# Kernel optimization log

Measured on AMD Instinct MI355X. Metric: run time of the kernel, lower is better.

The kernel has to match this reference:

```python
import jax, jax.numpy as jnp
import numpy as np

N, C, HD = 8192, 1024, 128

def setup_inputs() -> dict:
    key = jax.random.key(0)
    ks = jax.random.split(key, 9)
    def xavier(k, fan_in, fan_out):
        lim = float(np.sqrt(6.0 / (fan_in + fan_out)))
        return jax.random.uniform(k, (fan_out, fan_in), jnp.float32, -lim, lim)
    return {
        "x": jax.random.normal(ks[0], (N, C), jnp.float32),
        "Wq": xavier(ks[1], C, HD), "bq": jnp.zeros((HD,), jnp.float32),
        "Wk": xavier(ks[2], C, HD), "bk": jnp.zeros((HD,), jnp.float32),
        "Wv": xavier(ks[3], C, C),  "bv": jnp.zeros((C,), jnp.float32),
        "Wo": xavier(ks[4], C, C),  "bo": jnp.zeros((C,), jnp.float32),
    }

def reference(x, Wq, bq, Wk, bk, Wv, bv, Wo, bo):
    scale = HD ** -0.5
    q = x @ Wq.T + bq          # (N, HD)
    k = x @ Wk.T + bk          # (N, HD)
    v = x @ Wv.T + bv          # (N, C)
    scores = (q @ k.T) * scale # (N, N)
    attn = jax.nn.softmax(scores, axis=-1)
    out = attn @ v             # (N, C)
    return out @ Wo.T + bo
```

## Files before the change

### kernel.cpp

```cpp
#include <hip/hip_runtime.h>

#define NTOK 8192
#define CDIM 1024
#define HDIM 128

typedef __attribute__((ext_vector_type(8))) short short8;
typedef __attribute__((ext_vector_type(4))) float floatx4;
typedef __attribute__((ext_vector_type(16))) float floatx16;

__device__ inline unsigned short f2bf(float f) {
    union { float f; unsigned u; } v; v.f = f;
    unsigned r = v.u + 0x7fffu + ((v.u >> 16) & 1u);
    return (unsigned short)(r >> 16);
}
__device__ inline float bf2f(short s) {
    union { unsigned u; float f; } v;
    v.u = ((unsigned)(unsigned short)s) << 16;
    return v.f;
}
__device__ inline void async16(const unsigned short* g, short* l) {
    __builtin_amdgcn_global_load_lds(
        (const __attribute__((address_space(1))) unsigned*)g,
        (__attribute__((address_space(3))) unsigned*)l, 16, 0, 0);
}

__global__ void cast_f32_bf16(const float* __restrict__ in,
                              unsigned short* __restrict__ out, int n4) {
    int i = blockIdx.x * blockDim.x + threadIdx.x;
    if (i < n4) {
        float4 v = ((const float4*)in)[i];
        ushort4 o;
        o.x = f2bf(v.x); o.y = f2bf(v.y); o.z = f2bf(v.z); o.w = f2bf(v.w);
        ((ushort4*)out)[i] = o;
    }
}

template<int SWZ>
__global__ __launch_bounds__(256) void gemm_nt(
    const unsigned short* __restrict__ A, const unsigned short* __restrict__ W,
    const float* __restrict__ bias, unsigned short* __restrict__ out, int M, int N, int K)
{
    __shared__ short As[4][64][8];
    __shared__ short Ws[4][64][8];
    const int tid = threadIdx.x;
    const int wave = tid >> 6, lane = tid & 63;
    const int lr = lane & 15, lc = lane >> 4;
    const int m0 = blockIdx.x * 64, n0 = blockIdx.y * 64;

    floatx4 acc[4] = {};
    const int srow = tid >> 2, sch = tid & 3;
    const unsigned short* Ag = A + (long)(m0 + srow) * K + sch * 8;
    const unsigned short* Wg = W + (long)(n0 + srow) * K + sch * 8;

    for (int k0 = 0; k0 < K; k0 += 32) {
        *(short8*)&As[sch][srow][0] = *(const short8*)(Ag + k0);
        *(short8*)&Ws[sch][srow][0] = *(const short8*)(Wg + k0);
        __syncthreads();
        short8 a = *(short8*)&As[lc][wave * 16 + lr][0];
#pragma unroll
        for (int s = 0; s < 4; s++) {
            short8 b = *(short8*)&Ws[lc][s * 16 + lr][0];
            acc[s] = __builtin_amdgcn_mfma_f32_16x16x32_bf16(a, b, acc[s], 0, 0, 0);
        }
        __syncthreads();
    }

#pragma unroll
    for (int s = 0; s < 4; s++) {
        int h = n0 + s * 16 + lr;
        float bv = bias[h];
        int tok0 = m0 + wave * 16 + lc * 4;
#pragma unroll
        for (int r = 0; r < 4; r++) {
            int tok = tok0 + r;
            if (SWZ)
                out[(tok >> 5) * 4096 + (h >> 3) * 256 + (tok & 31) * 8 + (h & 7)] =
                    f2bf(acc[s][r] + bv);
            else
                out[(long)tok * N + h] = f2bf(acc[s][r] + bv);
        }
    }
}

template<int MODE>
__global__ __launch_bounds__(256) void gemm128_nt(
    const unsigned short* __restrict__ A, const unsigned short* __restrict__ W,
    const float* __restrict__ bias, void* __restrict__ out, int M, int N, int K)
{
    __shared__ short As[128][4][8];
    __shared__ short Ws[128][4][8];
    const int tid = threadIdx.x, wave = tid >> 6, lane = tid & 63;
    const int lr = lane & 15, lc = lane >> 4;
    const int wm = (wave >> 1) * 64, wn = (wave & 1) * 64;
    const int m0 = blockIdx.x * 128, n0 = blockIdx.y * 128;

    floatx4 acc[4][4] = {};

    const int srow = lane >> 2, sch = lane & 3;
    const unsigned short* Ag0 = A + (long)(m0 + wave * 32 + srow) * K + sch * 8;
    const unsigned short* Ag1 = Ag0 + (long)16 * K;
    const unsigned short* Wg0 = W + (long)(n0 + wave * 32 + srow) * K + sch * 8;
    const unsigned short* Wg1 = Wg0 + (long)16 * K;
    short* lA0 = &As[wave * 32][0][0];
    short* lA1 = &As[wave * 32 + 16][0][0];
    short* lW0 = &Ws[wave * 32][0][0];
    short* lW1 = &Ws[wave * 32 + 16][0][0];

    for (int k0 = 0; k0 < K; k0 += 32) {
        async16(Ag0 + k0, lA0);
        async16(Ag1 + k0, lA1);
        async16(Wg0 + k0, lW0);
        async16(Wg1 + k0, lW1);
        __syncthreads();
        short8 af[4], bfg[4];
#pragma unroll
        for (int i = 0; i < 4; i++) af[i]  = *(short8*)&As[wm + i * 16 + lr][lc][0];
#pragma unroll
        for (int j = 0; j < 4; j++) bfg[j] = *(short8*)&Ws[wn + j * 16 + lr][lc][0];
#pragma unroll
        for (int i = 0; i < 4; i++)
#pragma unroll
            for (int j = 0; j < 4; j++)
                acc[i][j] = __builtin_amdgcn_mfma_f32_16x16x32_bf16(af[i], bfg[j], acc[i][j], 0, 0, 0);
        __syncthreads();
    }

#pragma unroll
    for (int i = 0; i < 4; i++) {
        int t0 = m0 + wm + i * 16 + lc * 4;
#pragma unroll
        for (int j = 0; j < 4; j++) {
            int c = n0 + wn + j * 16 + lr;
            float bv = bias[c];
            if (MODE == 0) {
                float* o = (float*)out;
#pragma unroll
                for (int r = 0; r < 4; r++) o[(long)(t0 + r) * N + c] = acc[i][j][r] + bv;
            } else {
                unsigned short* o = (unsigned short*)out;
                ushort4 pk;
                pk.x = f2bf(acc[i][j][0] + bv); pk.y = f2bf(acc[i][j][1] + bv);
                pk.z = f2bf(acc[i][j][2] + bv); pk.w = f2bf(acc[i][j][3] + bv);
                long off = (long)(c >> 8) * 2097152 + (t0 >> 5) * 8192 +
                           ((t0 & 31) >> 3) * 2048 + (c & 255) * 8 + (t0 & 7);
                *(ushort4*)&o[off] = pk;
            }
        }
    }
}

__global__ __launch_bounds__(256, 2) void attn_pv(
    const unsigned short* __restrict__ qb, const unsigned short* __restrict__ ksw,
    const unsigned short* __restrict__ vsw,
    unsigned short* __restrict__ Oa, unsigned short* __restrict__ Ob,
    float* __restrict__ la, float* __restrict__ lb)
{
    __shared__ short Ks[3][16][32][8];
    __shared__ short Vs[3][4][256][8];

    const int tid = threadIdx.x, wave = tid >> 6, lane = tid & 63;
    const int l31 = lane & 31, h = lane >> 5;
    const int m0 = blockIdx.x * 128, cblk = blockIdx.y;
    const int mw = m0 + wave * 32;
    const int nt0 = blockIdx.z * 128;
    unsigned short* Op = blockIdx.z ? Ob : Oa;
    float* ls = blockIdx.z ? lb : la;
    const float cexp = (float)(0.08838834764831845 * 1.4426950408889634);

    short8 qf[8];
#pragma unroll
    for (int kk = 0; kk < 8; kk++)
        qf[kk] = *(const short8*)&qb[(mw + l31) * HDIM + kk * 16 + h * 8];

    floatx16 acc[8] = {};
    float ls0 = 0.f, ls1 = 0.f, ls2 = 0.f, ls3 = 0.f;

    const unsigned short* kg[2];
#pragma unroll
    for (int t = 0; t < 2; t++) kg[t] = ksw + (wave * 2 + t) * 512 + lane * 8;
    const unsigned short* vg[4];
#pragma unroll
    for (int t = 0; t < 4; t++)
        vg[t] = vsw + (long)cblk * 2097152 + (wave * 4 + t) * 512 + lane * 8;

    short* kr = &Ks[0][0][0][0];
    short* kn = &Ks[1][0][0][0];
    short* kw = &Ks[2][0][0][0];
    short* vr = &Vs[0][0][0][0];
    short* vn = &Vs[1][0][0][0];
    short* vw = &Vs[2][0][0][0];

#define STAGE(NT, KD, VD)                                               \
    {                                                                   \
        long nt_ = (NT);                                                \
        async16(kg[0] + nt_ * 4096, (KD) + (wave * 2 + 0) * 512);       \
        async16(kg[1] + nt_ * 4096, (KD) + (wave * 2 + 1) * 512);       \
        async16(vg[0] + nt_ * 8192, (VD) + (wave * 4 + 0) * 512);       \
        async16(vg[1] + nt_ * 8192, (VD) + (wave * 4 + 1) * 512);       \
        async16(vg[2] + nt_ * 8192, (VD) + (wave * 4 + 2) * 512);       \
        async16(vg[3] + nt_ * 8192, (VD) + (wave * 4 + 3) * 512);       \
    }

    STAGE(nt0, kr, vr);
    STAGE(nt0 + 1, kn, vn);

    for (int it = 0; it < 128; ++it) {
        if (it == 127) asm volatile("s_waitcnt vmcnt(0)" ::: "memory");
        else           asm volatile("s_waitcnt vmcnt(6)" ::: "memory");
        __builtin_amdgcn_sched_barrier(0);
        __builtin_amdgcn_s_barrier();
        __builtin_amdgcn_sched_barrier(0);
        if (it + 2 < 128) STAGE(nt0 + it + 2, kw, vw);
        __builtin_amdgcn_sched_barrier(0);

        floatx16 st = {};
        __builtin_amdgcn_s_setprio(1);
#pragma unroll
        for (int kk = 0; kk < 8; kk++) {
            short8 kf = *(short8*)(kr + (kk * 2 + h) * 256 + l31 * 8);
            st = __builtin_amdgcn_mfma_f32_32x32x16_bf16(kf, qf[kk], st, 0, 0, 0);
        }
        __builtin_amdgcn_s_setprio(0);

        unsigned pk0, pk1, pk2, pk3, pk4, pk5, pk6, pk7;
        {
            float p0, p1;
#define PK(I, DST, LS) \
            p0 = __builtin_amdgcn_exp2f(st[2 * I] * cexp); \
            p1 = __builtin_amdgcn_exp2f(st[2 * I + 1] * cexp); \
            LS += p0 + p1; \
            asm("v_cvt_pk_bf16_f32 %0, %1, %2" : "=v"(DST) : "v"(p0), "v"(p1));
            PK(0, pk0, ls0) PK(1, pk1, ls1) PK(2, pk2, ls2) PK(3, pk3, ls3)
            PK(4, pk4, ls0) PK(5, pk5, ls1) PK(6, pk6, ls2) PK(7, pk7, ls3)
#undef PK
        }
        asm("v_permlane32_swap_b32 %0, %1" : "+v"(pk0), "+v"(pk2));
        asm("v_permlane32_swap_b32 %0, %1" : "+v"(pk1), "+v"(pk3));
        asm("v_permlane32_swap_b32 %0, %1" : "+v"(pk4), "+v"(pk6));
        asm("v_permlane32_swap_b32 %0, %1" : "+v"(pk5), "+v"(pk7));
        union { unsigned u[4]; short8 s; } up0, up1;
        up0.u[0] = pk0; up0.u[1] = pk1; up0.u[2] = pk2; up0.u[3] = pk3;
        up1.u[0] = pk4; up1.u[1] = pk5; up1.u[2] = pk6; up1.u[3] = pk7;
        const short8 pa0 = up0.s, pa1 = up1.s;

        __builtin_amdgcn_s_setprio(1);
#pragma unroll
        for (int ct = 0; ct < 8; ct++) {
            short8 bv0 = *(short8*)(vr + h * 2048 + (ct * 32 + l31) * 8);
            short8 bv1 = *(short8*)(vr + (2 + h) * 2048 + (ct * 32 + l31) * 8);
            acc[ct] = __builtin_amdgcn_mfma_f32_32x32x16_bf16(pa0, bv0, acc[ct], 0, 0, 0);
            acc[ct] = __builtin_amdgcn_mfma_f32_32x32x16_bf16(pa1, bv1, acc[ct], 0, 0, 0);
        }
        __builtin_amdgcn_s_setprio(0);

        short* t0 = kr; kr = kn; kn = kw; kw = t0;
        short* t1 = vr; vr = vn; vn = vw; vw = t1;
    }
#undef STAGE

#pragma unroll
    for (int ct = 0; ct < 8; ct++) {
        int c = cblk * 256 + ct * 32 + l31;
#pragma unroll
        for (int r = 0; r < 16; r++) {
            int q = (r & 3) + 8 * (r >> 2) + 4 * h;
            Op[(long)(mw + q) * CDIM + c] = f2bf(acc[ct][r]);
        }
    }
    if (blockIdx.y == 0) {
        float lsum = (ls0 + ls1) + (ls2 + ls3);
        lsum += __shfl_xor(lsum, 32);
        if (lane < 32) ls[mw + lane] = lsum;
    }
}

__global__ __launch_bounds__(256) void combine_attn(
    const unsigned short* __restrict__ Oa, unsigned short* __restrict__ Ob,
    const float* __restrict__ la, const float* __restrict__ lb)
{
    int i = blockIdx.x * blockDim.x + threadIdx.x;
    int row = i >> 7;
    float inv = 1.0f / (la[row] + lb[row]);
    short8 a = ((const short8*)Oa)[i];
    short8 b = ((const short8*)Ob)[i];
    short8 o;
#pragma unroll
    for (int e = 0; e < 8; e++) o[e] = (short)f2bf((bf2f(a[e]) + bf2f(b[e])) * inv);
    ((short8*)Ob)[i] = o;
}

extern "C" void kernel_launch(void* const* d_in, const int* in_sizes, int n_in,
                              void* d_out, int out_size, void* d_ws, size_t ws_size,
                              hipStream_t stream) {
    const float* x  = (const float*)d_in[0];
    const float* Wq = (const float*)d_in[1];
    const float* bq = (const float*)d_in[2];
    const float* Wk = (const float*)d_in[3];
    const float* bk = (const float*)d_in[4];
    const float* Wv = (const float*)d_in[5];
    const float* bv = (const float*)d_in[6];
    const float* Wo = (const float*)d_in[7];
    const float* bo = (const float*)d_in[8];

    char* ws = (char*)d_ws;
    unsigned short* x_bf   = (unsigned short*)(ws + 0);
    unsigned short* wq_bf  = (unsigned short*)(ws + 16777216);
    unsigned short* wk_bf  = (unsigned short*)(ws + 17039360);
    unsigned short* wv_bf  = (unsigned short*)(ws + 17301504);
    unsigned short* wo_bf  = (unsigned short*)(ws + 19398656);
    unsigned short* q_bf   = (unsigned short*)(ws + 21495808);
    unsigned short* k_swz  = (unsigned short*)(ws + 23592960);
    unsigned short* v_swz  = (unsigned short*)(ws + 25690112);
    unsigned short* attn_bf= (unsigned short*)(ws + 42467328);
    float* lsum_a          = (float*)(ws + 59244544);
    float* lsum_b          = (float*)(ws + 59277312);

    cast_f32_bf16<<<8192, 256, 0, stream>>>(x,  x_bf,  2097152);
    cast_f32_bf16<<<128,  256, 0, stream>>>(Wq, wq_bf, 32768);
    cast_f32_bf16<<<128,  256, 0, stream>>>(Wk, wk_bf, 32768);
    cast_f32_bf16<<<1024, 256, 0, stream>>>(Wv, wv_bf, 262144);
    cast_f32_bf16<<<1024, 256, 0, stream>>>(Wo, wo_bf, 262144);

    gemm_nt<0><<<dim3(128, 2), 256, 0, stream>>>(x_bf, wq_bf, bq, q_bf, NTOK, HDIM, CDIM);
    gemm_nt<1><<<dim3(128, 2), 256, 0, stream>>>(x_bf, wk_bf, bk, k_swz, NTOK, HDIM, CDIM);
    gemm128_nt<2><<<dim3(64, 8), 256, 0, stream>>>(x_bf, wv_bf, bv, v_swz, NTOK, CDIM, CDIM);

    attn_pv<<<dim3(64, 4, 2), 256, 0, stream>>>(q_bf, k_swz, v_swz,
                                                x_bf, attn_bf, lsum_a, lsum_b);
    combine_attn<<<4096, 256, 0, stream>>>(x_bf, attn_bf, lsum_a, lsum_b);

    gemm128_nt<0><<<dim3(64, 8), 256, 0, stream>>>(attn_bf, wo_bf, bo, d_out, NTOK, CDIM, CDIM);
}
```

Measured before the change: 396.1 us.

## Widen attention blocks to 8 waves with two-tile stages; fuse Q/K projection launches

The attention kernel now runs 512-thread blocks covering 256 query rows. Each pipeline stage loads two key/value tiles into a 3-slot LDS ring, and the next stage is prefetched before the wait. Sharing each K/V tile across 8 waves halves the global-to-LDS traffic per query row and halves the number of barriers. The cost is about 144KB of LDS per block, which forces one block per CU and leaves a shallower prefetch distance. The Q and K projection GEMMs are also merged into one launch to save a kernel launch.

```diff
diff --git a/kernel.cpp b/kernel.cpp
--- a/kernel.cpp
+++ b/kernel.cpp
@@ -35,17 +35,22 @@
     }
 }
 
-template<int SWZ>
-__global__ __launch_bounds__(256) void gemm_nt(
-    const unsigned short* __restrict__ A, const unsigned short* __restrict__ W,
-    const float* __restrict__ bias, unsigned short* __restrict__ out, int M, int N, int K)
+__global__ __launch_bounds__(256) void gemm_qk(
+    const unsigned short* __restrict__ A,
+    const unsigned short* __restrict__ Wq, const float* __restrict__ bq,
+    const unsigned short* __restrict__ Wk, const float* __restrict__ bk,
+    unsigned short* __restrict__ qout, unsigned short* __restrict__ kout, int K)
 {
     __shared__ short As[4][64][8];
     __shared__ short Ws[4][64][8];
     const int tid = threadIdx.x;
     const int wave = tid >> 6, lane = tid & 63;
     const int lr = lane & 15, lc = lane >> 4;
-    const int m0 = blockIdx.x * 64, n0 = blockIdx.y * 64;
+    const int m0 = blockIdx.x * 64;
+    const int isK = blockIdx.y >> 1;
+    const int n0 = (blockIdx.y & 1) * 64;
+    const unsigned short* W = isK ? Wk : Wq;
+    const float* bias = isK ? bk : bq;
 
     floatx4 acc[4] = {};
     const int srow = tid >> 2, sch = tid & 3;
@@ -73,11 +78,11 @@
 #pragma unroll
         for (int r = 0; r < 4; r++) {
             int tok = tok0 + r;
-            if (SWZ)
-                out[(tok >> 5) * 4096 + (h >> 3) * 256 + (tok & 31) * 8 + (h & 7)] =
+            if (isK)
+                kout[(tok >> 5) * 4096 + (h >> 3) * 256 + (tok & 31) * 8 + (h & 7)] =
                     f2bf(acc[s][r] + bv);
             else
-                out[(long)tok * N + h] = f2bf(acc[s][r] + bv);
+                qout[(long)tok * HDIM + h] = f2bf(acc[s][r] + bv);
         }
     }
 }
@@ -149,18 +154,18 @@
     }
 }
 
-__global__ __launch_bounds__(256, 2) void attn_pv(
+__global__ __launch_bounds__(512, 2) void attn_pv(
     const unsigned short* __restrict__ qb, const unsigned short* __restrict__ ksw,
     const unsigned short* __restrict__ vsw,
     unsigned short* __restrict__ Oa, unsigned short* __restrict__ Ob,
     float* __restrict__ la, float* __restrict__ lb)
 {
-    __shared__ short Ks[3][16][32][8];
-    __shared__ short Vs[3][4][256][8];
+    __shared__ short Ks[3][8192];
+    __shared__ short Vs[3][16384];
 
     const int tid = threadIdx.x, wave = tid >> 6, lane = tid & 63;
     const int l31 = lane & 31, h = lane >> 5;
-    const int m0 = blockIdx.x * 128, cblk = blockIdx.y;
+    const int m0 = blockIdx.x * 256, cblk = blockIdx.y;
     const int mw = m0 + wave * 32;
     const int nt0 = blockIdx.z * 128;
     unsigned short* Op = blockIdx.z ? Ob : Oa;
@@ -175,86 +180,92 @@
     floatx16 acc[8] = {};
     float ls0 = 0.f, ls1 = 0.f, ls2 = 0.f, ls3 = 0.f;
 
-    const unsigned short* kg[2];
-#pragma unroll
-    for (int t = 0; t < 2; t++) kg[t] = ksw + (wave * 2 + t) * 512 + lane * 8;
-    const unsigned short* vg[4];
-#pragma unroll
-    for (int t = 0; t < 4; t++)
-        vg[t] = vsw + (long)cblk * 2097152 + (wave * 4 + t) * 512 + lane * 8;
-
-    short* kr = &Ks[0][0][0][0];
-    short* kn = &Ks[1][0][0][0];
-    short* kw = &Ks[2][0][0][0];
-    short* vr = &Vs[0][0][0][0];
-    short* vn = &Vs[1][0][0][0];
-    short* vw = &Vs[2][0][0][0];
-
-#define STAGE(NT, KD, VD)                                               \
+    const unsigned short* kg0 = ksw + (wave * 2 + 0) * 512 + lane * 8;
+    const unsigned short* kg1 = ksw + (wave * 2 + 1) * 512 + lane * 8;
+    const unsigned short* vgb = vsw + (long)cblk * 2097152 + lane * 8;
+    const unsigned short* vg0 = vgb + (wave * 4 + 0) * 512;
+    const unsigned short* vg1 = vgb + (wave * 4 + 1) * 512;
+    const unsigned short* vg2 = vgb + (wave * 4 + 2) * 512;
+    const unsigned short* vg3 = vgb + (wave * 4 + 3) * 512;
+
+    short* kr = &Ks[0][0];
+    short* kw = &Ks[1][0];
+    short* k2 = &Ks[2][0];
+    short* vr = &Vs[0][0];
+    short* vw = &Vs[1][0];
+    short* v2 = &Vs[2][0];
+
+#define STAGE(P, KD, VD)                                                \
     {                                                                   \
-        long nt_ = (NT);                                                \
-        async16(kg[0] + nt_ * 4096, (KD) + (wave * 2 + 0) * 512);       \
-        async16(kg[1] + nt_ * 4096, (KD) + (wave * 2 + 1) * 512);       \
-        async16(vg[0] + nt_ * 8192, (VD) + (wave * 4 + 0) * 512);       \
-        async16(vg[1] + nt_ * 8192, (VD) + (wave * 4 + 1) * 512);       \
-        async16(vg[2] + nt_ * 8192, (VD) + (wave * 4 + 2) * 512);       \
-        async16(vg[3] + nt_ * 8192, (VD) + (wave * 4 + 3) * 512);       \
-    }
-
-    STAGE(nt0, kr, vr);
-    STAGE(nt0 + 1, kn, vn);
-
-    for (int it = 0; it < 128; ++it) {
-        if (it == 127) asm volatile("s_waitcnt vmcnt(0)" ::: "memory");
-        else           asm volatile("s_waitcnt vmcnt(6)" ::: "memory");
+        long ok_ = (long)(nt0 + 2 * (P)) * 4096;                        \
+        long ov_ = (long)(nt0 + 2 * (P)) * 8192;                        \
+        async16(kg0 + ok_, (KD) + (wave * 2 + 0) * 512);                \
+        async16(kg1 + ok_, (KD) + (wave * 2 + 1) * 512);                \
+        async16(vg0 + ov_, (VD) + (wave * 4 + 0) * 512);                \
+        async16(vg1 + ov_, (VD) + (wave * 4 + 1) * 512);                \
+        async16(vg2 + ov_, (VD) + (wave * 4 + 2) * 512);                \
+        async16(vg3 + ov_, (VD) + (wave * 4 + 3) * 512);                \
+    }
+
+    STAGE(0, kr, vr);
+
+    for (int p = 0; p < 64; ++p) {
+        if (p + 1 < 64) STAGE(p + 1, kw, vw);
+        __builtin_amdgcn_sched_barrier(0);
+        if (p == 63) asm volatile("s_waitcnt vmcnt(0)" ::: "memory");
+        else         asm volatile("s_waitcnt vmcnt(6)" ::: "memory");
         __builtin_amdgcn_sched_barrier(0);
         __builtin_amdgcn_s_barrier();
         __builtin_amdgcn_sched_barrier(0);
-        if (it + 2 < 128) STAGE(nt0 + it + 2, kw, vw);
-        __builtin_amdgcn_sched_barrier(0);
-
-        floatx16 st = {};
-        __builtin_amdgcn_s_setprio(1);
-#pragma unroll
-        for (int kk = 0; kk < 8; kk++) {
-            short8 kf = *(short8*)(kr + (kk * 2 + h) * 256 + l31 * 8);
-            st = __builtin_amdgcn_mfma_f32_32x32x16_bf16(kf, qf[kk], st, 0, 0, 0);
-        }
-        __builtin_amdgcn_s_setprio(0);
-
-        unsigned pk0, pk1, pk2, pk3, pk4, pk5, pk6, pk7;
-        {
-            float p0, p1;
+
+#pragma unroll
+        for (int t = 0; t < 2; t++) {
+            short* kb = kr + t * 4096;
+            short* vb = vr + t * 8192;
+
+            floatx16 st = {};
+            __builtin_amdgcn_s_setprio(1);
+#pragma unroll
+            for (int kk = 0; kk < 8; kk++) {
+                short8 kf = *(short8*)(kb + (kk * 2 + h) * 256 + l31 * 8);
+                st = __builtin_amdgcn_mfma_f32_32x32x16_bf16(kf, qf[kk], st, 0, 0, 0);
+            }
+            __builtin_amdgcn_s_setprio(0);
+
+            unsigned pk0, pk1, pk2, pk3, pk4, pk5, pk6, pk7;
+            {
+                float p0, p1;
 #define PK(I, DST, LS) \
-            p0 = __builtin_amdgcn_exp2f(st[2 * I] * cexp); \
-            p1 = __builtin_amdgcn_exp2f(st[2 * I + 1] * cexp); \
-            LS += p0 + p1; \
-            asm("v_cvt_pk_bf16_f32 %0, %1, %2" : "=v"(DST) : "v"(p0), "v"(p1));
-            PK(0, pk0, ls0) PK(1, pk1, ls1) PK(2, pk2, ls2) PK(3, pk3, ls3)
-            PK(4, pk4, ls0) PK(5, pk5, ls1) PK(6, pk6, ls2) PK(7, pk7, ls3)
+                p0 = __builtin_amdgcn_exp2f(st[2 * I] * cexp); \
+                p1 = __builtin_amdgcn_exp2f(st[2 * I + 1] * cexp); \
+                LS += p0 + p1; \
+                asm("v_cvt_pk_bf16_f32 %0, %1, %2" : "=v"(DST) : "v"(p0), "v"(p1));
+                PK(0, pk0, ls0) PK(1, pk1, ls1) PK(2, pk2, ls2) PK(3, pk3, ls3)
+                PK(4, pk4, ls0) PK(5, pk5, ls1) PK(6, pk6, ls2) PK(7, pk7, ls3)
 #undef PK
-        }
-        asm("v_permlane32_swap_b32 %0, %1" : "+v"(pk0), "+v"(pk2));
-        asm("v_permlane32_swap_b32 %0, %1" : "+v"(pk1), "+v"(pk3));
-        asm("v_permlane32_swap_b32 %0, %1" : "+v"(pk4), "+v"(pk6));
-        asm("v_permlane32_swap_b32 %0, %1" : "+v"(pk5), "+v"(pk7));
-        union { unsigned u[4]; short8 s; } up0, up1;
-        up0.u[0] = pk0; up0.u[1] = pk1; up0.u[2] = pk2; up0.u[3] = pk3;
-        up1.u[0] = pk4; up1.u[1] = pk5; up1.u[2] = pk6; up1.u[3] = pk7;
-        const short8 pa0 = up0.s, pa1 = up1.s;
-
-        __builtin_amdgcn_s_setprio(1);
-#pragma unroll
-        for (int ct = 0; ct < 8; ct++) {
-            short8 bv0 = *(short8*)(vr + h * 2048 + (ct * 32 + l31) * 8);
-            short8 bv1 = *(short8*)(vr + (2 + h) * 2048 + (ct * 32 + l31) * 8);
-            acc[ct] = __builtin_amdgcn_mfma_f32_32x32x16_bf16(pa0, bv0, acc[ct], 0, 0, 0);
-            acc[ct] = __builtin_amdgcn_mfma_f32_32x32x16_bf16(pa1, bv1, acc[ct], 0, 0, 0);
-        }
-        __builtin_amdgcn_s_setprio(0);
-
-        short* t0 = kr; kr = kn; kn = kw; kw = t0;
-        short* t1 = vr; vr = vn; vn = vw; vw = t1;
+            }
+            asm("v_permlane32_swap_b32 %0, %1" : "+v"(pk0), "+v"(pk2));
+            asm("v_permlane32_swap_b32 %0, %1" : "+v"(pk1), "+v"(pk3));
+            asm("v_permlane32_swap_b32 %0, %1" : "+v"(pk4), "+v"(pk6));
+            asm("v_permlane32_swap_b32 %0, %1" : "+v"(pk5), "+v"(pk7));
+            union { unsigned u[4]; short8 s; } up0, up1;
+            up0.u[0] = pk0; up0.u[1] = pk1; up0.u[2] = pk2; up0.u[3] = pk3;
+            up1.u[0] = pk4; up1.u[1] = pk5; up1.u[2] = pk6; up1.u[3] = pk7;
+            const short8 pa0 = up0.s, pa1 = up1.s;
+
+            __builtin_amdgcn_s_setprio(1);
+#pragma unroll
+            for (int ct = 0; ct < 8; ct++) {
+                short8 bv0 = *(short8*)(vb + h * 2048 + (ct * 32 + l31) * 8);
+                short8 bv1 = *(short8*)(vb + (2 + h) * 2048 + (ct * 32 + l31) * 8);
+                acc[ct] = __builtin_amdgcn_mfma_f32_32x32x16_bf16(pa0, bv0, acc[ct], 0, 0, 0);
+                acc[ct] = __builtin_amdgcn_mfma_f32_32x32x16_bf16(pa1, bv1, acc[ct], 0, 0, 0);
+            }
+            __builtin_amdgcn_s_setprio(0);
+        }
+
+        short* t0 = kr; kr = kw; kw = k2; k2 = t0;
+        short* t1 = vr; vr = vw; vw = v2; v2 = t1;
     }
 #undef STAGE
 
@@ -321,11 +332,11 @@
     cast_f32_bf16<<<1024, 256, 0, stream>>>(Wv, wv_bf, 262144);
     cast_f32_bf16<<<1024, 256, 0, stream>>>(Wo, wo_bf, 262144);
 
-    gemm_nt<0><<<dim3(128, 2), 256, 0, stream>>>(x_bf, wq_bf, bq, q_bf, NTOK, HDIM, CDIM);
-    gemm_nt<1><<<dim3(128, 2), 256, 0, stream>>>(x_bf, wk_bf, bk, k_swz, NTOK, HDIM, CDIM);
+    gemm_qk<<<dim3(128, 4), 256, 0, stream>>>(x_bf, wq_bf, bq, wk_bf, bk,
+                                              q_bf, k_swz, CDIM);
     gemm128_nt<2><<<dim3(64, 8), 256, 0, stream>>>(x_bf, wv_bf, bv, v_swz, NTOK, CDIM, CDIM);
 
-    attn_pv<<<dim3(64, 4, 2), 256, 0, stream>>>(q_bf, k_swz, v_swz,
+    attn_pv<<<dim3(32, 4, 2), 512, 0, stream>>>(q_bf, k_swz, v_swz,
                                                 x_bf, attn_bf, lsum_a, lsum_b);
     combine_attn<<<4096, 256, 0, stream>>>(x_bf, attn_bf, lsum_a, lsum_b);
 
```

New measurement: 373.3 us. 1.06x faster.
